# Optimization experiments

Measured on AMD Instinct MI355X. Metric: run time of the kernel, lower is better.

Reference implementation:

```python
import jax, jax.numpy as jnp
from jax import lax
import numpy as np

B, N = 32, 16384
C, K = 64, 21
T = 30
L = 10.0
LAM = 0.1


def setup_inputs() -> dict:
    key = jax.random.key(0)
    k1, k2 = jax.random.split(key)
    y = jax.random.normal(k1, (B, 1, N), dtype=jnp.float32)
    H = jax.random.normal(k2, (C, 1, K), dtype=jnp.float32)
    H = H / jnp.linalg.norm(H, axis=-1, keepdims=True)  # F.normalize(p=2, dim=-1)
    return {"y": y, "H": H}


def _conv(y, H):
    # torch F.conv1d(y [B,1,N], H [C,1,K]) -> [B,C,N-K+1] (cross-correlation)
    return lax.conv_general_dilated(y, H, (1,), 'VALID',
                                    dimension_numbers=('NCH', 'OIH', 'NCH'))


def _convT(x, H):
    # torch F.conv_transpose1d(x [B,C,M], H [C,1,K]) -> [B,1,M+K-1]
    k = H.shape[-1]
    Ht = jnp.transpose(jnp.flip(H, -1), (1, 0, 2))  # [1,C,K] OIH, flipped
    return lax.conv_general_dilated(x, Ht, (1,), [(k - 1, k - 1)],
                                    dimension_numbers=('NCH', 'OIH', 'NCH'))


def reference(y, H):
    enc_dim = y.shape[-1] - H.shape[-1] + 1  # N - K + 1
    b = y.shape[0]
    c = H.shape[0]
    x0 = jnp.zeros((b, c, enc_dim), dtype=y.dtype)
    s0 = jnp.asarray(1.0, dtype=y.dtype)

    def step(carry, _):
        x_old, x_tmp, s_old = carry
        res = y - _convT(x_tmp, H)                      # residual [B,1,N]
        x_new = x_tmp + _conv(res, H) / L               # gradient step
        x_new = jax.nn.relu(x_new - LAM / L)            # soft-threshold (nonneg)
        s_new = (1.0 + jnp.sqrt(1.0 + 4.0 * s_old * s_old)) / 2.0
        x_tmp_next = x_new + (s_old - 1.0) / s_new * (x_new - x_old)
        return (x_new, x_tmp_next, s_new), None

    (x_new, _, _), _ = lax.scan(step, (x0, x0, s0), None, length=T)
    y_hat = _convT(x_new, H)
    return (y_hat, x_new)
```

## Files before the change

kernel.cpp:

```cpp
#include <hip/hip_runtime.h>
#include <math.h>

#define B_ 32
#define N_ 16384
#define K_ 21
#define C_ 64
#define M_ (N_ - K_ + 1)
#define T_ 30

#define TILE 236
#define NBLK 70
#define UPW  256
#define XRW  280
#define NT   256

__global__ __launch_bounds__(NT) void fused_step2_kernel(
    const float* __restrict__ Xc, const float* __restrict__ Xo,
    float* __restrict__ Xw,
    const float* __restrict__ Ut, const float* __restrict__ Uo,
    float* __restrict__ Uw,
    const float* __restrict__ y, const float* __restrict__ Hg,
    const float bp, const float bm, const int first)
{
  __shared__ float rs[256];
  __shared__ float xr[16][XRW];
  __shared__ float rp[4][256];

  const int tid = threadIdx.x;
  const int wv  = tid >> 6;
  const int l   = tid & 63;
  const int b   = blockIdx.y;
  const int x   = blockIdx.x;
  const int m0  = x * TILE;
  const bool has_o = (bm != 0.f);

  {
    float4* p = (float4*)&xr[0][0];
    #pragma unroll
    for (int s = 0; s < 5; ++s) {
      const int idx = tid + (s << 8);
      if (idx < 16 * XRW / 4) p[idx] = make_float4(0.f, 0.f, 0.f, 0.f);
    }
  }

  {
    const int n = m0 + tid;
    float r = 0.f;
    if (n < N_) {
      r = y[(size_t)b * N_ + n];
      if (!first) {
        const float* Ub = Ut + (size_t)b * NBLK * UPW;
        float ut;
        if (tid >= 236) {
          ut = Ub[(x + 1) * UPW + tid - 236] + Ub[x * UPW + tid];
        } else {
          ut = Ub[x * UPW + tid];
          if (tid < 20 && x > 0) ut += Ub[(x - 1) * UPW + 236 + tid];
        }
        r -= bp * ut;
        if (has_o) {
          const float* Vb = Uo + (size_t)b * NBLK * UPW;
          float uo;
          if (tid >= 236) {
            uo = Vb[(x + 1) * UPW + tid - 236] + Vb[x * UPW + tid];
          } else {
            uo = Vb[x * UPW + tid];
            if (tid < 20 && x > 0) uo += Vb[(x - 1) * UPW + 236 + tid];
          }
          r -= bm * uo;
        }
      }
    }
    rs[tid] = r;
  }
  __syncthreads();

  const int rem = M_ - m0;
  const bool act = (l < 59) && ((l << 2) < rem);
  float p0 = 0.f, p1 = 0.f, p2 = 0.f, p3 = 0.f;

  for (int k = 0; k < 4; ++k) {
    if (act) {
      float wr[24];
      #pragma unroll
      for (int kk = 0; kk < 6; ++kk) {
        const float4 v = *(const float4*)&rs[(l << 2) + (kk << 2)];
        wr[4*kk+0] = v.x; wr[4*kk+1] = v.y;
        wr[4*kk+2] = v.z; wr[4*kk+3] = v.w;
      }
      #pragma unroll
      for (int j = 0; j < 4; ++j) {
        const int row = (wv << 2) + j;
        const int cg  = __builtin_amdgcn_readfirstlane((k << 4) + row);
        const size_t gro = ((size_t)b * C_ + cg) * M_ + m0 + (l << 2);
        float xt0 = 0.f, xt1 = 0.f, xt2 = 0.f, xt3 = 0.f;
        if (!first) {
          const float4 a = *(const float4*)(Xc + gro);
          float ox = 0.f, oy = 0.f, oz = 0.f, ow = 0.f;
          if (has_o) {
            const float4 o = *(const float4*)(Xo + gro);
            ox = o.x; oy = o.y; oz = o.z; ow = o.w;
          }
          xt0 = fmaf(bm, ox, bp * a.x);
          xt1 = fmaf(bm, oy, bp * a.y);
          xt2 = fmaf(bm, oz, bp * a.z);
          xt3 = fmaf(bm, ow, bp * a.w);
        }
        const float* hc = Hg + cg * K_;
        float g0 = 0.f, g1 = 0.f, g2 = 0.f, g3 = 0.f;
        #pragma unroll
        for (int u = 0; u < 21; ++u) {
          const float hv = hc[u];
          g0 = fmaf(wr[u],     hv, g0);
          g1 = fmaf(wr[u + 1], hv, g1);
          g2 = fmaf(wr[u + 2], hv, g2);
          g3 = fmaf(wr[u + 3], hv, g3);
        }
        const float o0 = fmaxf(fmaf(g0, 0.1f, xt0) - 0.01f, 0.f);
        const float o1 = fmaxf(fmaf(g1, 0.1f, xt1) - 0.01f, 0.f);
        const float o2 = fmaxf(fmaf(g2, 0.1f, xt2) - 0.01f, 0.f);
        const float o3 = fmaxf(fmaf(g3, 0.1f, xt3) - 0.01f, 0.f);
        *(float4*)(Xw + gro) = make_float4(o0, o1, o2, o3);
        *(float4*)&xr[row][20 + (l << 2)] = make_float4(o0, o1, o2, o3);
      }
    }
    __syncthreads();

    #pragma unroll
    for (int j = 0; j < 4; ++j) {
      const int row = (wv << 2) + j;
      const int cg  = __builtin_amdgcn_readfirstlane((k << 4) + row);
      const float* hc = Hg + cg * K_;
      float w[24];
      #pragma unroll
      for (int kk = 0; kk < 6; ++kk) {
        const float4 v = *(const float4*)&xr[row][(l << 2) + (kk << 2)];
        w[4*kk+0] = v.x; w[4*kk+1] = v.y;
        w[4*kk+2] = v.z; w[4*kk+3] = v.w;
      }
      #pragma unroll
      for (int u = 0; u < 21; ++u) {
        const float hv = hc[20 - u];
        p0 = fmaf(w[u],     hv, p0);
        p1 = fmaf(w[u + 1], hv, p1);
        p2 = fmaf(w[u + 2], hv, p2);
        p3 = fmaf(w[u + 3], hv, p3);
      }
    }
    __syncthreads();
  }

  rp[wv][(l<<2)+0] = p0; rp[wv][(l<<2)+1] = p1;
  rp[wv][(l<<2)+2] = p2; rp[wv][(l<<2)+3] = p3;
  __syncthreads();

  Uw[((size_t)b * NBLK + x) * UPW + tid] =
      rp[0][tid] + rp[1][tid] + rp[2][tid] + rp[3][tid];
}

__global__ __launch_bounds__(NT) void yhat_combine_kernel(
    const float* __restrict__ Uw, float* __restrict__ outy)
{
  const int tid = threadIdx.x;
  const int n = blockIdx.x * 256 + tid;
  const int b = blockIdx.y;
  const int x = n / 236;
  const int i = n - x * 236;
  const float* Ub = Uw + (size_t)b * NBLK * UPW;
  float v = Ub[x * UPW + i];
  if (i < 20 && x > 0) v += Ub[(x - 1) * UPW + 236 + i];
  outy[(size_t)b * N_ + n] = v;
}

#define XWID 276
#define Q4PC 69
#define NQ4  (16 * Q4PC)

__global__ __launch_bounds__(NT, 4) void fused_step_r5_kernel(
    const float* __restrict__ Xc, const float* __restrict__ Xo,
    float* __restrict__ Xw, const float* __restrict__ y,
    const float* __restrict__ Hg, const float bp, const float bm,
    const int first)
{
  __shared__ float xs[16][XWID];
  __shared__ float rp[4][256];
  __shared__ float rs[256];

  const int tid = threadIdx.x;
  const int wv  = tid >> 6;
  const int l   = tid & 63;
  const int b   = blockIdx.y;
  const int m0  = blockIdx.x * TILE;
  const int g0  = m0 - 20;
  const bool has_o = (bm != 0.f);

  if (!first) {
    float p0 = 0.f, p1 = 0.f, p2 = 0.f, p3 = 0.f;
    for (int k = 0; k < 4; ++k) {
      const int ch0 = k << 4;
      const float* pcb = Xc + ((size_t)b * C_ + ch0) * M_;
      const float* pob = Xo + ((size_t)b * C_ + ch0) * M_;
      __syncthreads();
      for (int f = tid; f < NQ4; f += NT) {
        const int c  = f / Q4PC;
        const int i4 = f - c * Q4PC;
        const int g  = g0 + (i4 << 2);
        const float* pa = pcb + (size_t)c * M_ + g;
        const float* pb = pob + (size_t)c * M_ + g;
        float ax, ay, az, aw, ox, oy, oz, ow;
        if (g >= 0 && g + 3 < M_) {
          const float4 a = *(const float4*)pa;
          ax = a.x; ay = a.y; az = a.z; aw = a.w;
          if (has_o) {
            const float4 o = *(const float4*)pb;
            ox = o.x; oy = o.y; oz = o.z; ow = o.w;
          } else { ox = oy = oz = ow = 0.f; }
        } else {
          ax = ay = az = aw = ox = oy = oz = ow = 0.f;
          if ((unsigned)(g+0) < (unsigned)M_) { ax = pa[0]; if (has_o) ox = pb[0]; }
          if ((unsigned)(g+1) < (unsigned)M_) { ay = pa[1]; if (has_o) oy = pb[1]; }
          if ((unsigned)(g+2) < (unsigned)M_) { az = pa[2]; if (has_o) oz = pb[2]; }
          if ((unsigned)(g+3) < (unsigned)M_) { aw = pa[3]; if (has_o) ow = pb[3]; }
        }
        float4 w4;
        w4.x = fmaf(bm, ox, bp * ax);
        w4.y = fmaf(bm, oy, bp * ay);
        w4.z = fmaf(bm, oz, bp * az);
        w4.w = fmaf(bm, ow, bp * aw);
        *(float4*)&xs[c][i4 << 2] = w4;
      }
      __syncthreads();
      #pragma unroll
      for (int j = 0; j < 4; ++j) {
        const int cloc = (wv << 2) + j;
        const int cg = __builtin_amdgcn_readfirstlane(ch0 + cloc);
        const float* hc = Hg + cg * K_;
        float w[24];
        #pragma unroll
        for (int kk = 0; kk < 6; ++kk) {
          const float4 v = *(const float4*)&xs[cloc][(l << 2) + (kk << 2)];
          w[4*kk+0] = v.x; w[4*kk+1] = v.y;
          w[4*kk+2] = v.z; w[4*kk+3] = v.w;
        }
        #pragma unroll
        for (int u = 0; u < 21; ++u) {
          const float hv = hc[20 - u];
          p0 = fmaf(w[u],     hv, p0);
          p1 = fmaf(w[u + 1], hv, p1);
          p2 = fmaf(w[u + 2], hv, p2);
          p3 = fmaf(w[u + 3], hv, p3);
        }
      }
    }
    *(float4*)&rp[wv][l << 2] = make_float4(p0, p1, p2, p3);
  }
  __syncthreads();

  {
    const int n = m0 + tid;
    float r = 0.f;
    if (n < N_) {
      r = y[(size_t)b * N_ + n];
      if (!first) r -= rp[0][tid] + rp[1][tid] + rp[2][tid] + rp[3][tid];
    }
    rs[tid] = r;
  }
  __syncthreads();

  if (l < 59 && (l << 2) < M_ - m0) {
    float wr[24];
    #pragma unroll
    for (int kk = 0; kk < 6; ++kk) {
      const float4 v = *(const float4*)&rs[(l << 2) + (kk << 2)];
      wr[4*kk+0] = v.x; wr[4*kk+1] = v.y;
      wr[4*kk+2] = v.z; wr[4*kk+3] = v.w;
    }
    #pragma unroll 4
    for (int cl = 0; cl < 16; ++cl) {
      const int cg = __builtin_amdgcn_readfirstlane((wv << 4) + cl);
      const size_t row = ((size_t)b * C_ + cg) * M_ + m0 + (l << 2);
      float xt0, xt1, xt2, xt3;
      if (!first) {
        const float4 a = *(const float4*)(Xc + row);
        float ox = 0.f, oy = 0.f, oz = 0.f, ow = 0.f;
        if (has_o) {
          const float4 o = *(const float4*)(Xo + row);
          ox = o.x; oy = o.y; oz = o.z; ow = o.w;
        }
        xt0 = fmaf(bm, ox, bp * a.x);
        xt1 = fmaf(bm, oy, bp * a.y);
        xt2 = fmaf(bm, oz, bp * a.z);
        xt3 = fmaf(bm, ow, bp * a.w);
      } else { xt0 = xt1 = xt2 = xt3 = 0.f; }
      const float* hc = Hg + cg * K_;
      float a0 = 0.f, a1 = 0.f, a2 = 0.f, a3 = 0.f;
      #pragma unroll
      for (int u = 0; u < 21; ++u) {
        const float hv = hc[u];
        a0 = fmaf(wr[u],     hv, a0);
        a1 = fmaf(wr[u + 1], hv, a1);
        a2 = fmaf(wr[u + 2], hv, a2);
        a3 = fmaf(wr[u + 3], hv, a3);
      }
      const float o0 = fmaxf(fmaf(a0, 0.1f, xt0) - 0.01f, 0.f);
      const float o1 = fmaxf(fmaf(a1, 0.1f, xt1) - 0.01f, 0.f);
      const float o2 = fmaxf(fmaf(a2, 0.1f, xt2) - 0.01f, 0.f);
      const float o3 = fmaxf(fmaf(a3, 0.1f, xt3) - 0.01f, 0.f);
      *(float4*)(Xw + row) = make_float4(o0, o1, o2, o3);
    }
  }
}

#define TA 1024
#define CC 16

__global__ __launch_bounds__(NT) void convT_kernel(
    const float* __restrict__ X, const float* __restrict__ y,
    const float* __restrict__ Hg, float* __restrict__ out,
    const int use_y, const float sign)
{
  __shared__ float xs[CC][TA + 20];
  __shared__ float hs[C_][K_];
  const int tid = threadIdx.x;
  const int b = blockIdx.y;
  const int n0 = blockIdx.x * TA;

  for (int f = tid; f < C_ * K_; f += NT) hs[f / K_][f % K_] = sign * Hg[f];

  float acc[4];
  if (use_y) {
    const float4 v = *(const float4*)(y + (size_t)b * N_ + n0 + tid * 4);
    acc[0] = v.x; acc[1] = v.y; acc[2] = v.z; acc[3] = v.w;
  } else {
    acc[0] = acc[1] = acc[2] = acc[3] = 0.f;
  }
  const bool interior = (n0 >= 20) && (n0 + TA - 1 <= M_ - 1);
  const int QROW = (TA + 20) / 4;
  for (int cb = 0; cb < C_; cb += CC) {
    __syncthreads();
    for (int f = tid; f < CC * QROW; f += NT) {
      const int c = f / QROW;
      const int i = (f % QROW) * 4;
      const int gx = n0 - 20 + i;
      const float* src = X + ((size_t)(b * C_ + cb + c)) * M_ + gx;
      float4 v;
      if (interior) {
        v = *(const float4*)src;
      } else {
        v.x = (gx >= 0     && gx < M_)     ? src[0] : 0.f;
        v.y = (gx + 1 >= 0 && gx + 1 < M_) ? src[1] : 0.f;
        v.z = (gx + 2 >= 0 && gx + 2 < M_) ? src[2] : 0.f;
        v.w = (gx + 3 >= 0 && gx + 3 < M_) ? src[3] : 0.f;
      }
      *(float4*)&xs[c][i] = v;
    }
    __syncthreads();
    for (int c = 0; c < CC; ++c) {
      float w[24];
      #pragma unroll
      for (int k = 0; k < 6; ++k) {
        const float4 v = *(const float4*)&xs[c][tid * 4 + k * 4];
        w[k*4] = v.x; w[k*4+1] = v.y; w[k*4+2] = v.z; w[k*4+3] = v.w;
      }
      const float* hr = hs[cb + c];
      #pragma unroll
      for (int j = 0; j < K_; ++j) {
        const float h = hr[j];
        acc[0] = fmaf(h, w[20 - j], acc[0]);
        acc[1] = fmaf(h, w[21 - j], acc[1]);
        acc[2] = fmaf(h, w[22 - j], acc[2]);
        acc[3] = fmaf(h, w[23 - j], acc[3]);
      }
    }
  }
  *(float4*)(out + (size_t)b * N_ + n0 + tid * 4) =
      make_float4(acc[0], acc[1], acc[2], acc[3]);
}

extern "C" void kernel_launch(void* const* d_in, const int* in_sizes, int n_in,
                              void* d_out, int out_size, void* d_ws, size_t ws_size,
                              hipStream_t stream)
{
  const float* y = (const float*)d_in[0];
  const float* H = (const float*)d_in[1];
  float* out  = (float*)d_out;
  float* outy = out;
  float* outx = out + (size_t)B_ * N_;

  const size_t SZ = (size_t)B_ * C_ * M_;
  const size_t UP = (size_t)B_ * NBLK * UPW;

  float betas[T_];
  double s = 1.0;
  for (int t = 0; t < T_; ++t) {
    const double sn = (1.0 + sqrt(1.0 + 4.0 * s * s)) * 0.5;
    betas[t] = (float)((s - 1.0) / sn);
    s = sn;
  }

  float* P[3] = { (float*)d_ws, (float*)d_ws + SZ, outx };
  const dim3 blk(NT);

  if (ws_size >= (2 * SZ + 3 * UP) * sizeof(float)) {
    float* U[3] = { (float*)d_ws + 2 * SZ,
                    (float*)d_ws + 2 * SZ + UP,
                    (float*)d_ws + 2 * SZ + 2 * UP };
    const dim3 gF(NBLK, B_);
    for (int t = 0; t < T_; ++t) {
      const float beta = (t >= 1) ? betas[t - 1] : 0.f;
      const float* Xc = P[(t + 2) % 3];
      const float* Xo = (beta != 0.f) ? P[(t + 1) % 3] : P[(t + 2) % 3];
      float*       Xw = P[t % 3];
      const float* Ut = U[(t + 2) % 3];
      const float* Uo = (beta != 0.f) ? U[(t + 1) % 3] : U[(t + 2) % 3];
      float*       Uw = U[t % 3];
      fused_step2_kernel<<<gF, blk, 0, stream>>>(
          Xc, Xo, Xw, Ut, Uo, Uw, y, H, 1.f + beta, -beta, t == 0);
    }
    const dim3 gY(N_ / 256, B_);
    yhat_combine_kernel<<<gY, blk, 0, stream>>>(U[(T_ - 1) % 3], outy);
  } else {
    const dim3 gF((M_ + TILE - 1) / TILE, B_);
    for (int t = 0; t < T_; ++t) {
      const float beta = (t >= 1) ? betas[t - 1] : 0.f;
      const float* Xc = P[(t + 2) % 3];
      const float* Xo = (beta != 0.f) ? P[(t + 1) % 3] : P[(t + 2) % 3];
      float*       Xw = P[t % 3];
      fused_step_r5_kernel<<<gF, blk, 0, stream>>>(Xc, Xo, Xw, y, H,
                                                   1.f + beta, -beta, t == 0);
    }
    const dim3 gA(N_ / TA, B_);
    convT_kernel<<<gA, blk, 0, stream>>>(outx, y, H, outy, 0, 1.f);
  }
}
```

Measured before the change: 2.995 ms.

## Replace shared-memory x tile exchange with wavefront shuffles and drop barriers

Each channel's freshly thresholded x values are now passed between lanes with __shfl instead of being written to a 16-row shared-memory tile and read back. This removes the xr shared buffer, its zero-initialisation, and both per-k-iteration __syncthreads, and hoists the residual window load out of the channel loop. All lanes now compute, with inactive lanes clamped to a safe address and zeroed, so the shuffles see defined values. The cost is 20 shuffles per channel and some wasted work on idle lanes (l>=59).

```diff
diff --git a/kernel.cpp b/kernel.cpp
--- a/kernel.cpp
+++ b/kernel.cpp
@@ -11,10 +11,9 @@
 #define TILE 236
 #define NBLK 70
 #define UPW  256
-#define XRW  280
 #define NT   256
 
-__global__ __launch_bounds__(NT) void fused_step2_kernel(
+__global__ __launch_bounds__(NT) void fused_step4_kernel(
     const float* __restrict__ Xc, const float* __restrict__ Xo,
     float* __restrict__ Xw,
     const float* __restrict__ Ut, const float* __restrict__ Uo,
@@ -22,8 +21,7 @@
     const float* __restrict__ y, const float* __restrict__ Hg,
     const float bp, const float bm, const int first)
 {
-  __shared__ float rs[256];
-  __shared__ float xr[16][XRW];
+  __shared__ float rs[280];
   __shared__ float rp[4][256];
 
   const int tid = threadIdx.x;
@@ -34,14 +32,7 @@
   const int m0  = x * TILE;
   const bool has_o = (bm != 0.f);
 
-  {
-    float4* p = (float4*)&xr[0][0];
-    #pragma unroll
-    for (int s = 0; s < 5; ++s) {
-      const int idx = tid + (s << 8);
-      if (idx < 16 * XRW / 4) p[idx] = make_float4(0.f, 0.f, 0.f, 0.f);
-    }
-  }
+  if (tid < 24) rs[256 + tid] = 0.f;
 
   {
     const int n = m0 + tid;
@@ -75,69 +66,75 @@
   }
   __syncthreads();
 
-  const int rem = M_ - m0;
-  const bool act = (l < 59) && ((l << 2) < rem);
+  float wr[24];
+  #pragma unroll
+  for (int kk = 0; kk < 6; ++kk) {
+    const float4 v = *(const float4*)&rs[(l << 2) + (kk << 2)];
+    wr[4*kk+0] = v.x; wr[4*kk+1] = v.y;
+    wr[4*kk+2] = v.z; wr[4*kk+3] = v.w;
+  }
+
+  const int  mown = m0 + (l << 2);
+  const int  coff = (mown <= M_ - 4) ? mown : (M_ - 4);
+  const bool act  = (l < 59) && ((l << 2) < M_ - m0);
+  const size_t bC = (size_t)b * C_;
+
   float p0 = 0.f, p1 = 0.f, p2 = 0.f, p3 = 0.f;
 
   for (int k = 0; k < 4; ++k) {
-    if (act) {
-      float wr[24];
-      #pragma unroll
-      for (int kk = 0; kk < 6; ++kk) {
-        const float4 v = *(const float4*)&rs[(l << 2) + (kk << 2)];
-        wr[4*kk+0] = v.x; wr[4*kk+1] = v.y;
-        wr[4*kk+2] = v.z; wr[4*kk+3] = v.w;
-      }
-      #pragma unroll
-      for (int j = 0; j < 4; ++j) {
-        const int row = (wv << 2) + j;
-        const int cg  = __builtin_amdgcn_readfirstlane((k << 4) + row);
-        const size_t gro = ((size_t)b * C_ + cg) * M_ + m0 + (l << 2);
-        float xt0 = 0.f, xt1 = 0.f, xt2 = 0.f, xt3 = 0.f;
-        if (!first) {
-          const float4 a = *(const float4*)(Xc + gro);
-          float ox = 0.f, oy = 0.f, oz = 0.f, ow = 0.f;
-          if (has_o) {
-            const float4 o = *(const float4*)(Xo + gro);
-            ox = o.x; oy = o.y; oz = o.z; ow = o.w;
-          }
-          xt0 = fmaf(bm, ox, bp * a.x);
-          xt1 = fmaf(bm, oy, bp * a.y);
-          xt2 = fmaf(bm, oz, bp * a.z);
-          xt3 = fmaf(bm, ow, bp * a.w);
-        }
-        const float* hc = Hg + cg * K_;
-        float g0 = 0.f, g1 = 0.f, g2 = 0.f, g3 = 0.f;
-        #pragma unroll
-        for (int u = 0; u < 21; ++u) {
-          const float hv = hc[u];
-          g0 = fmaf(wr[u],     hv, g0);
-          g1 = fmaf(wr[u + 1], hv, g1);
-          g2 = fmaf(wr[u + 2], hv, g2);
-          g3 = fmaf(wr[u + 3], hv, g3);
-        }
-        const float o0 = fmaxf(fmaf(g0, 0.1f, xt0) - 0.01f, 0.f);
-        const float o1 = fmaxf(fmaf(g1, 0.1f, xt1) - 0.01f, 0.f);
-        const float o2 = fmaxf(fmaf(g2, 0.1f, xt2) - 0.01f, 0.f);
-        const float o3 = fmaxf(fmaf(g3, 0.1f, xt3) - 0.01f, 0.f);
-        *(float4*)(Xw + gro) = make_float4(o0, o1, o2, o3);
-        *(float4*)&xr[row][20 + (l << 2)] = make_float4(o0, o1, o2, o3);
-      }
-    }
-    __syncthreads();
-
     #pragma unroll
     for (int j = 0; j < 4; ++j) {
-      const int row = (wv << 2) + j;
-      const int cg  = __builtin_amdgcn_readfirstlane((k << 4) + row);
+      const int cg = __builtin_amdgcn_readfirstlane((k << 4) + (wv << 2) + j);
       const float* hc = Hg + cg * K_;
+
+      float g0 = 0.f, g1 = 0.f, g2 = 0.f, g3 = 0.f;
+      #pragma unroll
+      for (int u = 0; u < 21; ++u) {
+        const float hv = hc[u];
+        g0 = fmaf(wr[u],     hv, g0);
+        g1 = fmaf(wr[u + 1], hv, g1);
+        g2 = fmaf(wr[u + 2], hv, g2);
+        g3 = fmaf(wr[u + 3], hv, g3);
+      }
+
+      float xt0 = 0.f, xt1 = 0.f, xt2 = 0.f, xt3 = 0.f;
+      if (!first) {
+        const float4 a = *(const float4*)(Xc + (bC + cg) * M_ + coff);
+        float ox = 0.f, oy = 0.f, oz = 0.f, ow = 0.f;
+        if (has_o) {
+          const float4 o = *(const float4*)(Xo + (bC + cg) * M_ + coff);
+          ox = o.x; oy = o.y; oz = o.z; ow = o.w;
+        }
+        xt0 = fmaf(bm, ox, bp * a.x);
+        xt1 = fmaf(bm, oy, bp * a.y);
+        xt2 = fmaf(bm, oz, bp * a.z);
+        xt3 = fmaf(bm, ow, bp * a.w);
+      }
+
+      float o0 = fmaxf(fmaf(g0, 0.1f, xt0) - 0.01f, 0.f);
+      float o1 = fmaxf(fmaf(g1, 0.1f, xt1) - 0.01f, 0.f);
+      float o2 = fmaxf(fmaf(g2, 0.1f, xt2) - 0.01f, 0.f);
+      float o3 = fmaxf(fmaf(g3, 0.1f, xt3) - 0.01f, 0.f);
+      if (!act) { o0 = 0.f; o1 = 0.f; o2 = 0.f; o3 = 0.f; }
+      if (act)
+        *(float4*)(Xw + (bC + cg) * M_ + mown) = make_float4(o0, o1, o2, o3);
+
       float w[24];
-      #pragma unroll
-      for (int kk = 0; kk < 6; ++kk) {
-        const float4 v = *(const float4*)&xr[row][(l << 2) + (kk << 2)];
-        w[4*kk+0] = v.x; w[4*kk+1] = v.y;
-        w[4*kk+2] = v.z; w[4*kk+3] = v.w;
-      }
+      w[20] = o0; w[21] = o1; w[22] = o2; w[23] = o3;
+      #pragma unroll
+      for (int d = 0; d < 5; ++d) {
+        const int src = l - 5 + d;
+        const float s0 = __shfl(o0, src);
+        const float s1 = __shfl(o1, src);
+        const float s2 = __shfl(o2, src);
+        const float s3 = __shfl(o3, src);
+        const bool ok = (src >= 0);
+        w[4*d+0] = ok ? s0 : 0.f;
+        w[4*d+1] = ok ? s1 : 0.f;
+        w[4*d+2] = ok ? s2 : 0.f;
+        w[4*d+3] = ok ? s3 : 0.f;
+      }
+
       #pragma unroll
       for (int u = 0; u < 21; ++u) {
         const float hv = hc[20 - u];
@@ -147,7 +144,6 @@
         p3 = fmaf(w[u + 3], hv, p3);
       }
     }
-    __syncthreads();
   }
 
   rp[wv][(l<<2)+0] = p0; rp[wv][(l<<2)+1] = p1;
@@ -414,7 +410,7 @@
       const float* Ut = U[(t + 2) % 3];
       const float* Uo = (beta != 0.f) ? U[(t + 1) % 3] : U[(t + 2) % 3];
       float*       Uw = U[t % 3];
-      fused_step2_kernel<<<gF, blk, 0, stream>>>(
+      fused_step4_kernel<<<gF, blk, 0, stream>>>(
           Xc, Xo, Xw, Ut, Uo, Uw, y, H, 1.f + beta, -beta, t == 0);
     }
     const dim3 gY(N_ / 256, B_);
```

After: 2.978 ms. No clear change (-0.6%).
